# Kernel optimization log

Measured on AMD Instinct MI355X. Metric: run time of the kernel, lower is better.

## Reference

```python
import jax, jax.numpy as jnp
import numpy as np

N = 50000        # nodes
E = 800000       # edges
G = 256          # graphs in batch
DIMS = [128, 128, 64, 32]
BN_EPS = 1e-5
TEMP = 5.0


def setup_inputs() -> dict:
    key = jax.random.key(0)
    ks = iter(jax.random.split(key, 32))
    inp = {}
    inp["x"] = jax.random.normal(next(ks), (N, DIMS[0]), dtype=jnp.float32)
    inp["edge_index"] = jax.random.randint(next(ks), (2, E), 0, N)
    inp["batch"] = jnp.sort(jax.random.randint(next(ks), (N,), 0, G))
    for i in range(3):
        din, dout = DIMS[i], DIMS[i + 1]
        inp[f"W1_{i}"] = jax.random.normal(next(ks), (din, dout), dtype=jnp.float32) * 0.05
        inp[f"b1_{i}"] = jnp.zeros((dout,), jnp.float32)
        inp[f"W2_{i}"] = jax.random.normal(next(ks), (dout, dout), dtype=jnp.float32) * 0.05
        inp[f"b2_{i}"] = jnp.zeros((dout,), jnp.float32)
        inp[f"gamma_{i}"] = jnp.ones((dout,), jnp.float32)
        inp[f"beta_{i}"] = jnp.zeros((dout,), jnp.float32)
        inp[f"mean_{i}"] = jnp.zeros((dout,), jnp.float32)
        inp[f"var_{i}"] = jnp.ones((dout,), jnp.float32)
    inp["W_lin"] = jax.random.normal(next(ks), (DIMS[3], 1), dtype=jnp.float32) * 0.05
    inp["b_lin"] = jnp.zeros((1,), jnp.float32)
    return inp


def _gin_bn(x, src, dst, W1, b1, W2, b2, g, b, m, v):
    # GINConv with eps=0: h_i = MLP(x_i + sum_{j->i} x_j), then BatchNorm (eval)
    agg = jax.ops.segment_sum(x[src], dst, num_segments=N)  # [N, din]
    h = x + agg
    h = jnp.maximum(h @ W1 + b1, 0.0) @ W2 + b2             # 2-layer MLP
    return (h - m) * jax.lax.rsqrt(v + BN_EPS) * g + b


def reference(x, edge_index, batch,
              W1_0, b1_0, W2_0, b2_0, gamma_0, beta_0, mean_0, var_0,
              W1_1, b1_1, W2_1, b2_1, gamma_1, beta_1, mean_1, var_1,
              W1_2, b1_2, W2_2, b2_2, gamma_2, beta_2, mean_2, var_2,
              W_lin, b_lin):
    src, dst = edge_index[0], edge_index[1]
    layers = [
        (W1_0, b1_0, W2_0, b2_0, gamma_0, beta_0, mean_0, var_0),
        (W1_1, b1_1, W2_1, b2_1, gamma_1, beta_1, mean_1, var_1),
        (W1_2, b1_2, W2_2, b2_2, gamma_2, beta_2, mean_2, var_2),
    ]
    for i, p in enumerate(layers):
        x = _gin_bn(x, src, dst, *p)
        if i != len(layers) - 1:
            x = jnp.maximum(x, 0.0)  # relu; dropout is identity in eval mode
    logits = (x @ W_lin + b_lin) / TEMP                      # [N, 1]
    # per-graph (segment) softmax over nodes
    mx = jax.ops.segment_max(logits, batch, num_segments=G)  # [G, 1]
    e = jnp.exp(logits - mx[batch])
    s = jax.ops.segment_sum(e, batch, num_segments=G)        # [G, 1]
    return e / s[batch]
```

## Files before the change

### kernel.cpp

```cpp
#include <hip/hip_runtime.h>

#define NN 50000
#define NE 800000
#define NG 256
#define NB ((NN + 255) / 256)
#define N4 (NN * 128 / 4)
#define NQ (NE / 4)

typedef __attribute__((ext_vector_type(8))) short bf16x8;
typedef __attribute__((ext_vector_type(4))) float f32x4;

__device__ __forceinline__ unsigned short f2bf_rne(float f) {
    unsigned u = __float_as_uint(f);
    u += 0x7fffu + ((u >> 16) & 1u);
    return (unsigned short)(u >> 16);
}
#define BF2F_LO(u) __uint_as_float((u) << 16)
#define BF2F_HI(u) __uint_as_float((u) & 0xffff0000u)

__global__ void conv_hist(const float4* __restrict__ x, ushort4* __restrict__ xh,
                          const int4* __restrict__ dst4, int* __restrict__ deg,
                          int4* __restrict__ eoff4) {
    int i = blockIdx.x * 256 + threadIdx.x;
    if (i < N4) {
        float4 v = x[i];
        ushort4 o;
        o.x = f2bf_rne(v.x); o.y = f2bf_rne(v.y);
        o.z = f2bf_rne(v.z); o.w = f2bf_rne(v.w);
        xh[i] = o;
    }
    int wv = threadIdx.x >> 6, ln = threadIdx.x & 63;
    if (ln < 8) {
        int q = blockIdx.x * 32 + wv * 8 + ln;
        if (q < NQ) {
            int4 d = dst4[q];
            int o0 = atomicAdd(&deg[d.x], 1);
            int o1 = atomicAdd(&deg[d.y], 1);
            int o2 = atomicAdd(&deg[d.z], 1);
            int o3 = atomicAdd(&deg[d.w], 1);
            eoff4[q] = make_int4(o0, o1, o2, o3);
        }
    }
}

__global__ void block_scan(const int* __restrict__ deg, int* __restrict__ iscan,
                           int* __restrict__ bsum,
                           const float* __restrict__ W1, const float* __restrict__ W2,
                           const float* __restrict__ W3,
                           const float* __restrict__ W21, const float* __restrict__ W12,
                           unsigned short* __restrict__ W1t,
                           unsigned short* __restrict__ W2t,
                           unsigned short* __restrict__ W3t,
                           unsigned short* __restrict__ W21t,
                           unsigned short* __restrict__ W12t) {
    int gidx = blockIdx.x * 256 + threadIdx.x;
    if (gidx < 16384) {
        int n = gidx >> 7, k = gidx & 127;
        W1t[gidx] = f2bf_rne(W1[k * 128 + n]);
        W2t[gidx] = f2bf_rne(W2[k * 128 + n]);
    } else if (gidx < 24576) {
        int i2 = gidx - 16384;
        int n = i2 >> 7, k = i2 & 127;
        W3t[i2] = f2bf_rne(W3[k * 64 + n]);
    } else if (gidx < 28672) {
        int i3 = gidx - 24576;
        int n = i3 >> 6, k = i3 & 63;
        W21t[i3] = f2bf_rne(W21[k * 64 + n]);
    } else if (gidx < 30720) {
        int i4 = gidx - 28672;
        int n = i4 >> 6, k = i4 & 63;
        W12t[i4] = f2bf_rne(W12[k * 32 + n]);
    }

    __shared__ int sh[256];
    int t = threadIdx.x;
    int i = blockIdx.x * 256 + t;
    int v = (i < NN) ? deg[i] : 0;
    sh[t] = v;
    __syncthreads();
    #pragma unroll
    for (int off = 1; off < 256; off <<= 1) {
        int add = (t >= off) ? sh[t - off] : 0;
        __syncthreads();
        sh[t] += add;
        __syncthreads();
    }
    if (i < NN) iscan[i] = sh[t];
    if (t == 255) bsum[blockIdx.x] = sh[255];
}

__global__ void scan_bsum(const int* __restrict__ bsum, int* __restrict__ boff) {
    __shared__ int sh[256];
    int t = threadIdx.x;
    int v = (t < NB) ? bsum[t] : 0;
    sh[t] = v;
    __syncthreads();
    #pragma unroll
    for (int off = 1; off < 256; off <<= 1) {
        int add = (t >= off) ? sh[t - off] : 0;
        __syncthreads();
        sh[t] += add;
        __syncthreads();
    }
    if (t < NB) boff[t] = sh[t] - v;
}

__global__ void finalize_bounds(const int* __restrict__ deg, const int* __restrict__ iscan,
                                const int* __restrict__ boff, int* __restrict__ rowptr,
                                const int* __restrict__ batch, int* __restrict__ gstart) {
    int i = blockIdx.x * 256 + threadIdx.x;
    if (i < NN) {
        rowptr[i] = iscan[i] - deg[i] + boff[blockIdx.x];
        int b = batch[i];
        if (i == 0) {
            for (int g = 0; g <= b; g++) gstart[g] = 0;
        } else {
            int p = batch[i - 1];
            for (int g = p + 1; g <= b; g++) gstart[g] = i;
        }
        if (i == NN - 1) {
            for (int g = b + 1; g <= NG; g++) gstart[g] = NN;
        }
    }
    if (i == 0) rowptr[NN] = NE;
}

__global__ void fill_csr2(const int4* __restrict__ src4, const int4* __restrict__ dst4,
                          const int* __restrict__ rowptr, const int4* __restrict__ eoff4,
                          int* __restrict__ esrc) {
    int q = blockIdx.x * 256 + threadIdx.x;
    if (q >= NQ) return;
    int4 s = src4[q];
    int4 d = dst4[q];
    int4 o = eoff4[q];
    int r0 = rowptr[d.x];
    int r1 = rowptr[d.y];
    int r2 = rowptr[d.z];
    int r3 = rowptr[d.w];
    esrc[r0 + o.x] = s.x;
    esrc[r1 + o.y] = s.y;
    esrc[r2 + o.z] = s.z;
    esrc[r3 + o.w] = s.w;
}


template <int C4>
__device__ __forceinline__ void gather_bf16(const uint4* __restrict__ x4,
                                            const int* __restrict__ esrc,
                                            int beg, int cnt, int node, int lane,
                                            float* a ) {
    constexpr int EPI = 64 / C4;
    const int chunk = lane & (C4 - 1);
    const int esl   = lane / C4;
    #define ACC_U4(u) do { \
        a[0] += BF2F_LO((u).x); a[1] += BF2F_HI((u).x); \
        a[2] += BF2F_LO((u).y); a[3] += BF2F_HI((u).y); \
        a[4] += BF2F_LO((u).z); a[5] += BF2F_HI((u).z); \
        a[6] += BF2F_LO((u).w); a[7] += BF2F_HI((u).w); } while (0)
    if (esl == 0) { uint4 u = x4[(size_t)node * C4 + chunk]; ACC_U4(u); }
    for (int c = 0; c < cnt; c += 64) {
        int take = min(64, cnt - c);
        int myi = (lane < take) ? esrc[beg + c + lane] : 0;
        int i = 0;
        for (; i + 4 * EPI <= take; i += 4 * EPI) {
            int s0 = __shfl(myi, i + esl);
            int s1 = __shfl(myi, i + EPI + esl);
            int s2 = __shfl(myi, i + 2 * EPI + esl);
            int s3 = __shfl(myi, i + 3 * EPI + esl);
            uint4 u0 = x4[(size_t)s0 * C4 + chunk];
            uint4 u1 = x4[(size_t)s1 * C4 + chunk];
            uint4 u2 = x4[(size_t)s2 * C4 + chunk];
            uint4 u3 = x4[(size_t)s3 * C4 + chunk];
            ACC_U4(u0); ACC_U4(u1); ACC_U4(u2); ACC_U4(u3);
        }
        if (i + 2 * EPI <= take) {
            int s0 = __shfl(myi, i + esl);
            int s1 = __shfl(myi, i + EPI + esl);
            uint4 u0 = x4[(size_t)s0 * C4 + chunk];
            uint4 u1 = x4[(size_t)s1 * C4 + chunk];
            ACC_U4(u0); ACC_U4(u1);
            i += 2 * EPI;
        }
        if (i + EPI <= take) {
            int s = __shfl(myi, i + esl);
            uint4 u = x4[(size_t)s * C4 + chunk];
            ACC_U4(u);
            i += EPI;
        }
        int rem = take - i;
        if (rem > 0) {
            int s = __shfl(myi, i + ((esl < rem) ? esl : 0));
            uint4 u = x4[(size_t)s * C4 + chunk];
            if (esl < rem) ACC_U4(u);
        }
    }
    #undef ACC_U4
    for (int off = 32; off >= C4; off >>= 1) {
        #pragma unroll
        for (int q = 0; q < 8; q++)
            a[q] += __shfl_xor(a[q], off);
    }
}

template <int C>
__device__ __forceinline__ void gather_bf16_u2(const uint2* __restrict__ x2,
                                               const int* __restrict__ esrc,
                                               int beg, int cnt, int node, int lane,
                                               float* a ) {
    constexpr int EPI = 64 / C;
    const int chunk = lane & (C - 1);
    const int esl   = lane / C;
    #define ACC_U2(u) do { \
        a[0] += BF2F_LO((u).x); a[1] += BF2F_HI((u).x); \
        a[2] += BF2F_LO((u).y); a[3] += BF2F_HI((u).y); } while (0)
    if (esl == 0) { uint2 u = x2[(size_t)node * C + chunk]; ACC_U2(u); }
    for (int c = 0; c < cnt; c += 64) {
        int take = min(64, cnt - c);
        int myi = (lane < take) ? esrc[beg + c + lane] : 0;
        int i = 0;
        for (; i + 4 * EPI <= take; i += 4 * EPI) {
            int s0 = __shfl(myi, i + esl);
            int s1 = __shfl(myi, i + EPI + esl);
            int s2 = __shfl(myi, i + 2 * EPI + esl);
            int s3 = __shfl(myi, i + 3 * EPI + esl);
            uint2 u0 = x2[(size_t)s0 * C + chunk];
            uint2 u1 = x2[(size_t)s1 * C + chunk];
            uint2 u2 = x2[(size_t)s2 * C + chunk];
            uint2 u3 = x2[(size_t)s3 * C + chunk];
            ACC_U2(u0); ACC_U2(u1); ACC_U2(u2); ACC_U2(u3);
        }
        if (i + 2 * EPI <= take) {
            int s0 = __shfl(myi, i + esl);
            int s1 = __shfl(myi, i + EPI + esl);
            uint2 u0 = x2[(size_t)s0 * C + chunk];
            uint2 u1 = x2[(size_t)s1 * C + chunk];
            ACC_U2(u0); ACC_U2(u1);
            i += 2 * EPI;
        }
        if (i + EPI <= take) {
            int s = __shfl(myi, i + esl);
            uint2 u = x2[(size_t)s * C + chunk];
            ACC_U2(u);
            i += EPI;
        }
        int rem = take - i;
        if (rem > 0) {
            int s = __shfl(myi, i + ((esl < rem) ? esl : 0));
            uint2 u = x2[(size_t)s * C + chunk];
            if (esl < rem) ACC_U2(u);
        }
    }
    #undef ACC_U2
    for (int off = 32; off >= C; off >>= 1) {
        #pragma unroll
        for (int q = 0; q < 4; q++)
            a[q] += __shfl_xor(a[q], off);
    }
}

template <int C>
__device__ __forceinline__ void gather_bf16_u1(const unsigned* __restrict__ x1,
                                               const int* __restrict__ esrc,
                                               int beg, int cnt, int node, int lane,
                                               float* a ) {
    constexpr int EPI = 64 / C;
    const int chunk = lane & (C - 1);
    const int esl   = lane / C;
    #define ACC_U1(u) do { \
        a[0] += BF2F_LO(u); a[1] += BF2F_HI(u); } while (0)
    if (esl == 0) { unsigned u = x1[(size_t)node * C + chunk]; ACC_U1(u); }
    for (int c = 0; c < cnt; c += 64) {
        int take = min(64, cnt - c);
        int myi = (lane < take) ? esrc[beg + c + lane] : 0;
        int i = 0;
        for (; i + 4 * EPI <= take; i += 4 * EPI) {
            int s0 = __shfl(myi, i + esl);
            int s1 = __shfl(myi, i + EPI + esl);
            int s2 = __shfl(myi, i + 2 * EPI + esl);
            int s3 = __shfl(myi, i + 3 * EPI + esl);
            unsigned u0 = x1[(size_t)s0 * C + chunk];
            unsigned u1 = x1[(size_t)s1 * C + chunk];
            unsigned u2 = x1[(size_t)s2 * C + chunk];
            unsigned u3 = x1[(size_t)s3 * C + chunk];
            ACC_U1(u0); ACC_U1(u1); ACC_U1(u2); ACC_U1(u3);
        }
        if (i + 2 * EPI <= take) {
            int s0 = __shfl(myi, i + esl);
            int s1 = __shfl(myi, i + EPI + esl);
            unsigned u0 = x1[(size_t)s0 * C + chunk];
            unsigned u1 = x1[(size_t)s1 * C + chunk];
            ACC_U1(u0); ACC_U1(u1);
            i += 2 * EPI;
        }
        if (i + EPI <= take) {
            int s = __shfl(myi, i + esl);
            unsigned u = x1[(size_t)s * C + chunk];
            ACC_U1(u);
            i += EPI;
        }
        int rem = take - i;
        if (rem > 0) {
            int s = __shfl(myi, i + ((esl < rem) ? esl : 0));
            unsigned u = x1[(size_t)s * C + chunk];
            if (esl < rem) ACC_U1(u);
        }
    }
    #undef ACC_U1
    for (int off = 32; off >= C; off >>= 1) {
        #pragma unroll
        for (int q = 0; q < 2; q++)
            a[q] += __shfl_xor(a[q], off);
    }
}

__global__ __launch_bounds__(256) void gather_L0(
        const unsigned short* __restrict__ xh, const int* __restrict__ esrc,
        const int* __restrict__ rowptr, unsigned short* __restrict__ aggh ) {
    const int wave = threadIdx.x >> 6, lane = threadIdx.x & 63;
    const int node = blockIdx.x * 4 + wave;
    if (node >= NN) return;
    float a[8] = {0, 0, 0, 0, 0, 0, 0, 0};
    int beg = rowptr[node], end = rowptr[node + 1];
    gather_bf16<16>((const uint4*)xh, esrc, beg, end - beg, node, lane, a);
    if (lane < 16) {
        uint4 o;
        o.x = (unsigned)f2bf_rne(a[0]) | ((unsigned)f2bf_rne(a[1]) << 16);
        o.y = (unsigned)f2bf_rne(a[2]) | ((unsigned)f2bf_rne(a[3]) << 16);
        o.z = (unsigned)f2bf_rne(a[4]) | ((unsigned)f2bf_rne(a[5]) << 16);
        o.w = (unsigned)f2bf_rne(a[6]) | ((unsigned)f2bf_rne(a[7]) << 16);
        *(uint4*)&aggh[(size_t)node * 128 + lane * 8] = o;
    }
}

__global__ __launch_bounds__(256) void gather_L1(
        const unsigned short* __restrict__ z1h, const int* __restrict__ esrc,
        const int* __restrict__ rowptr, const float* __restrict__ b1,
        unsigned short* __restrict__ agg1h ) {
    const int wave = threadIdx.x >> 6, lane = threadIdx.x & 63;
    const int node = blockIdx.x * 4 + wave;
    if (node >= NN) return;
    float a[4] = {0, 0, 0, 0};
    int beg = rowptr[node], end = rowptr[node + 1];
    gather_bf16_u2<16>((const uint2*)z1h, esrc, beg, end - beg, node, lane, a);
    if (lane < 16) {
        float4 bv = *(const float4*)&b1[lane * 4];
        uint2 o;
        o.x = (unsigned)f2bf_rne(fmaxf(a[0] + bv.x, 0.f)) |
              ((unsigned)f2bf_rne(fmaxf(a[1] + bv.y, 0.f)) << 16);
        o.y = (unsigned)f2bf_rne(fmaxf(a[2] + bv.z, 0.f)) |
              ((unsigned)f2bf_rne(fmaxf(a[3] + bv.w, 0.f)) << 16);
        *(uint2*)&agg1h[(size_t)node * 64 + lane * 4] = o;
    }
}

__global__ __launch_bounds__(256) void gather_L2(
        const unsigned short* __restrict__ z2h, const int* __restrict__ esrc,
        const int* __restrict__ rowptr, const float* __restrict__ b1,
        unsigned short* __restrict__ agg2h ) {
    const int wave = threadIdx.x >> 6, lane = threadIdx.x & 63;
    const int node = blockIdx.x * 4 + wave;
    if (node >= NN) return;
    float a[2] = {0, 0};
    int beg = rowptr[node], end = rowptr[node + 1];
    gather_bf16_u1<16>((const unsigned*)z2h, esrc, beg, end - beg, node, lane, a);
    if (lane < 16) {
        float2 bv = *(const float2*)&b1[lane * 2];
        unsigned o = (unsigned)f2bf_rne(fmaxf(a[0] + bv.x, 0.f)) |
                     ((unsigned)f2bf_rne(fmaxf(a[1] + bv.y, 0.f)) << 16);
        *(unsigned*)&agg2h[(size_t)node * 32 + lane * 2] = o;
    }
}

__global__ __launch_bounds__(256) void gemm_L0(
        const unsigned short* __restrict__ aggh, unsigned short* __restrict__ z1h,
        const unsigned short* __restrict__ W1t,
        const unsigned short* __restrict__ W2t,
        const unsigned short* __restrict__ W3t,
        const float* __restrict__ b1, const float* __restrict__ b2,
        const float* __restrict__ gamma, const float* __restrict__ beta,
        const float* __restrict__ mean, const float* __restrict__ var) {
    constexpr int MT = 64, LDA = 136;
    __shared__ __align__(16) unsigned short shA[MT * LDA];
    __shared__ __align__(16) unsigned short shB[MT * LDA];
    const int tid = threadIdx.x;
    const int wave = tid >> 6, lane = tid & 63;
    const int nodeBase = blockIdx.x * MT;
    const int lr = lane & 15;
    const int lg = lane >> 4;
    const int lk = lg * 8;
    const int n0 = wave * 32;

    #pragma unroll
    for (int j = 0; j < 4; j++) {
        int f = tid + j * 256;
        int row = f >> 4, c = f & 15;
        int node = nodeBase + row;
        uint4 v = (node < NN) ? ((const uint4*)aggh)[(size_t)node * 16 + c]
                              : make_uint4(0u, 0u, 0u, 0u);
        *(uint4*)&shA[row * LDA + c * 8] = v;
    }
    __syncthreads();

    f32x4 acc[4][2];

    {
        float bv0 = b1[n0 + lr], bv1 = b1[n0 + 16 + lr];
        #pragma unroll
        for (int m = 0; m < 4; m++) {
            f32x4 c0 = {bv0, bv0, bv0, bv0};
            f32x4 c1 = {bv1, bv1, bv1, bv1};
            acc[m][0] = c0; acc[m][1] = c1;
        }
        #pragma unroll
        for (int ks = 0; ks < 4; ks++) {
            const int k0 = ks * 32 + lk;
            bf16x8 wb0 = *(const bf16x8*)&W1t[(n0 + lr) * 128 + k0];
            bf16x8 wb1 = *(const bf16x8*)&W1t[(n0 + 16 + lr) * 128 + k0];
            #pragma unroll
            for (int m = 0; m < 4; m++) {
                bf16x8 af = *(const bf16x8*)&shA[(m * 16 + lr) * LDA + k0];
                acc[m][0] = __builtin_amdgcn_mfma_f32_16x16x32_bf16(af, wb0, acc[m][0], 0, 0, 0);
                acc[m][1] = __builtin_amdgcn_mfma_f32_16x16x32_bf16(af, wb1, acc[m][1], 0, 0, 0);
            }
        }
    }
    #pragma unroll
    for (int m = 0; m < 4; m++) {
        #pragma unroll
        for (int nt = 0; nt < 2; nt++) {
            #pragma unroll
            for (int r = 0; r < 4; r++) {
                shB[(m * 16 + lg * 4 + r) * LDA + (n0 + nt * 16 + lr)] =
                    f2bf_rne(fmaxf(acc[m][nt][r], 0.f));
            }
        }
    }
    __syncthreads();

    {
        float bv0 = b2[n0 + lr], bv1 = b2[n0 + 16 + lr];
        #pragma unroll
        for (int m = 0; m < 4; m++) {
            f32x4 c0 = {bv0, bv0, bv0, bv0};
            f32x4 c1 = {bv1, bv1, bv1, bv1};
            acc[m][0] = c0; acc[m][1] = c1;
        }
        #pragma unroll
        for (int ks = 0; ks < 4; ks++) {
            const int k0 = ks * 32 + lk;
            bf16x8 wb0 = *(const bf16x8*)&W2t[(n0 + lr) * 128 + k0];
            bf16x8 wb1 = *(const bf16x8*)&W2t[(n0 + 16 + lr) * 128 + k0];
            #pragma unroll
            for (int m = 0; m < 4; m++) {
                bf16x8 af = *(const bf16x8*)&shB[(m * 16 + lr) * LDA + k0];
                acc[m][0] = __builtin_amdgcn_mfma_f32_16x16x32_bf16(af, wb0, acc[m][0], 0, 0, 0);
                acc[m][1] = __builtin_amdgcn_mfma_f32_16x16x32_bf16(af, wb1, acc[m][1], 0, 0, 0);
            }
        }
    }
    float s0 = gamma[n0 + lr]      * (1.0f / sqrtf(var[n0 + lr] + 1e-5f));
    float t0 = beta[n0 + lr]       - mean[n0 + lr] * s0;
    float s1 = gamma[n0 + 16 + lr] * (1.0f / sqrtf(var[n0 + 16 + lr] + 1e-5f));
    float t1 = beta[n0 + 16 + lr]  - mean[n0 + 16 + lr] * s1;
    #pragma unroll
    for (int m = 0; m < 4; m++) {
        #pragma unroll
        for (int nt = 0; nt < 2; nt++) {
            float sc = nt ? s1 : s0, sf = nt ? t1 : t0;
            #pragma unroll
            for (int r = 0; r < 4; r++) {
                float y = fmaxf(fmaf(acc[m][nt][r], sc, sf), 0.f);
                shA[(m * 16 + lg * 4 + r) * LDA + (n0 + nt * 16 + lr)] = f2bf_rne(y);
            }
        }
    }
    __syncthreads();

    f32x4 a3[4];
    #pragma unroll
    for (int m = 0; m < 4; m++) {
        f32x4 z = {0.f, 0.f, 0.f, 0.f};
        a3[m] = z;
    }
    #pragma unroll
    for (int ks = 0; ks < 4; ks++) {
        const int k0 = ks * 32 + lk;
        bf16x8 wb = *(const bf16x8*)&W3t[(wave * 16 + lr) * 128 + k0];
        #pragma unroll
        for (int m = 0; m < 4; m++) {
            bf16x8 af = *(const bf16x8*)&shA[(m * 16 + lr) * LDA + k0];
            a3[m] = __builtin_amdgcn_mfma_f32_16x16x32_bf16(af, wb, a3[m], 0, 0, 0);
        }
    }
    #pragma unroll
    for (int m = 0; m < 4; m++) {
        #pragma unroll
        for (int r = 0; r < 4; r++) {
            int node = nodeBase + m * 16 + lg * 4 + r;
            if (node < NN)
                z1h[(size_t)node * 64 + wave * 16 + lr] = f2bf_rne(a3[m][r]);
        }
    }
}

__global__ __launch_bounds__(256) void gemm_L1(
        const unsigned short* __restrict__ agg1h, unsigned short* __restrict__ z2h,
        const unsigned short* __restrict__ W21t,
        const unsigned short* __restrict__ W12t,
        const float* __restrict__ b2, const float* __restrict__ gamma,
        const float* __restrict__ beta, const float* __restrict__ mean,
        const float* __restrict__ var) {
    constexpr int MT = 64, LDA = 72;
    __shared__ __align__(16) unsigned short shA[MT * LDA];
    __shared__ __align__(16) unsigned short shB[MT * LDA];
    const int tid = threadIdx.x;
    const int wave = tid >> 6, lane = tid & 63;
    const int nodeBase = blockIdx.x * MT;
    const int lr = lane & 15;
    const int lg = lane >> 4;
    const int lk = lg * 8;
    const int n0 = wave * 16;

    #pragma unroll
    for (int j = 0; j < 2; j++) {
        int f = tid + j * 256;
        int row = f >> 3, c = f & 7;
        int node = nodeBase + row;
        uint4 v = (node < NN) ? ((const uint4*)agg1h)[(size_t)node * 8 + c]
                              : make_uint4(0u, 0u, 0u, 0u);
        *(uint4*)&shA[row * LDA + c * 8] = v;
    }
    __syncthreads();

    f32x4 acc[4];
    {
        float bv = b2[n0 + lr];
        #pragma unroll
        for (int m = 0; m < 4; m++) {
            f32x4 c0 = {bv, bv, bv, bv};
            acc[m] = c0;
        }
        #pragma unroll
        for (int ks = 0; ks < 2; ks++) {
            const int k0 = ks * 32 + lk;
            bf16x8 wb = *(const bf16x8*)&W21t[(n0 + lr) * 64 + k0];
            #pragma unroll
            for (int m = 0; m < 4; m++) {
                bf16x8 af = *(const bf16x8*)&shA[(m * 16 + lr) * LDA + k0];
                acc[m] = __builtin_amdgcn_mfma_f32_16x16x32_bf16(af, wb, acc[m], 0, 0, 0);
            }
        }
    }
    float sc = gamma[n0 + lr] * (1.0f / sqrtf(var[n0 + lr] + 1e-5f));
    float sf = beta[n0 + lr] - mean[n0 + lr] * sc;
    #pragma unroll
    for (int m = 0; m < 4; m++) {
        #pragma unroll
        for (int r = 0; r < 4; r++) {
            float y = fmaxf(fmaf(acc[m][r], sc, sf), 0.f);
            shB[(m * 16 + lg * 4 + r) * LDA + (n0 + lr)] = f2bf_rne(y);
        }
    }
    __syncthreads();

    const int rh = (wave >> 1) * 32, ch = (wave & 1) * 16;
    f32x4 a3[2];
    {
        f32x4 z = {0.f, 0.f, 0.f, 0.f};
        a3[0] = z; a3[1] = z;
    }
    #pragma unroll
    for (int ks = 0; ks < 2; ks++) {
        const int k0 = ks * 32 + lk;
        bf16x8 wb = *(const bf16x8*)&W12t[(ch + lr) * 64 + k0];
        #pragma unroll
        for (int m = 0; m < 2; m++) {
            bf16x8 af = *(const bf16x8*)&shB[(rh + m * 16 + lr) * LDA + k0];
            a3[m] = __builtin_amdgcn_mfma_f32_16x16x32_bf16(af, wb, a3[m], 0, 0, 0);
        }
    }
    #pragma unroll
    for (int m = 0; m < 2; m++) {
        #pragma unroll
        for (int r = 0; r < 4; r++) {
            int node = nodeBase + rh + m * 16 + lg * 4 + r;
            if (node < NN)
                z2h[(size_t)node * 32 + ch + lr] = f2bf_rne(a3[m][r]);
        }
    }
}

__global__ __launch_bounds__(256) void gemm_L2(
        const unsigned short* __restrict__ agg2h, float* __restrict__ logits,
        const float* __restrict__ W2, const float* __restrict__ b2,
        const float* __restrict__ gamma, const float* __restrict__ beta,
        const float* __restrict__ mean, const float* __restrict__ var,
        const float* __restrict__ Wl, const float* __restrict__ bl) {
    constexpr int MT = 32, LD = 36;
    __shared__ float sh[MT * LD];
    const int tid = threadIdx.x;
    const int nodeBase = blockIdx.x * MT;

    {
        int row = tid >> 3, c = tid & 7;
        int node = nodeBase + row;
        uint2 v = (node < NN) ? ((const uint2*)agg2h)[(size_t)node * 8 + c]
                              : make_uint2(0u, 0u);
        sh[row * LD + c * 4 + 0] = BF2F_LO(v.x);
        sh[row * LD + c * 4 + 1] = BF2F_HI(v.x);
        sh[row * LD + c * 4 + 2] = BF2F_LO(v.y);
        sh[row * LD + c * 4 + 3] = BF2F_HI(v.y);
    }
    __syncthreads();

    const int colid = tid % 8, rowid = tid / 8;
    const int c0 = colid * 4, r0 = rowid;
    float acc[4];
    {
        float4 bv = *(const float4*)&b2[c0];
        acc[0] = bv.x; acc[1] = bv.y; acc[2] = bv.z; acc[3] = bv.w;
        #pragma unroll
        for (int k4 = 0; k4 < 8; k4++) {
            float4 w[4];
            #pragma unroll
            for (int kk = 0; kk < 4; kk++)
                w[kk] = *(const float4*)&W2[(k4 * 4 + kk) * 32 + c0];
            float4 a = *(const float4*)&sh[r0 * LD + k4 * 4];
            const float av[4] = {a.x, a.y, a.z, a.w};
            #pragma unroll
            for (int kk = 0; kk < 4; kk++) {
                const float* wp = (const float*)&w[kk];
                #pragma unroll
                for (int j = 0; j < 4; j++)
                    acc[j] = fmaf(av[kk], wp[j], acc[j]);
            }
        }
    }
    float4 gv = *(const float4*)&gamma[c0];
    float4 bev = *(const float4*)&beta[c0];
    float4 mv = *(const float4*)&mean[c0];
    float4 vv = *(const float4*)&var[c0];
    float4 wl = *(const float4*)&Wl[c0];
    float p = 0.f;
    {
        const float* gp = (const float*)&gv; const float* bp = (const float*)&bev;
        const float* mp = (const float*)&mv; const float* vp = (const float*)&vv;
        const float* wp = (const float*)&wl;
        #pragma unroll
        for (int j = 0; j < 4; j++) {
            float sc = gp[j] * (1.0f / sqrtf(vp[j] + 1e-5f));
            float y = (acc[j] - mp[j]) * sc + bp[j];
            p = fmaf(y, wp[j], p);
        }
    }
    p += __shfl_xor(p, 1);
    p += __shfl_xor(p, 2);
    p += __shfl_xor(p, 4);
    int node = nodeBase + r0;
    if ((tid & 7) == 0 && node < NN)
        logits[node] = (p + bl[0]) * 0.2f;
}

__global__ __launch_bounds__(256) void seg_softmax(
        const float* __restrict__ logits, const int* __restrict__ gstart,
        float* __restrict__ out) {
    __shared__ float slog[1024];
    __shared__ float sred[4];
    __shared__ float sbc[2];
    int g = blockIdx.x;
    int beg = gstart[g], end = gstart[g + 1];
    int cnt = end - beg;
    int t = threadIdx.x;
    if (cnt <= 0) return;
    bool fits = (cnt <= 1024);

    float lmax = -3.402823466e+38f;
    for (int i = t; i < cnt; i += 256) {
        float lg = logits[beg + i];
        if (fits) slog[i] = lg;
        lmax = fmaxf(lmax, lg);
    }
    #pragma unroll
    for (int off = 32; off > 0; off >>= 1)
        lmax = fmaxf(lmax, __shfl_down(lmax, off));
    if ((t & 63) == 0) sred[t >> 6] = lmax;
    __syncthreads();
    if (t == 0) sbc[0] = fmaxf(fmaxf(sred[0], sred[1]), fmaxf(sred[2], sred[3]));
    __syncthreads();
    float gm = sbc[0];

    float lsum = 0.f;
    for (int i = t; i < cnt; i += 256) {
        float lg = fits ? slog[i] : logits[beg + i];
        float e = expf(lg - gm);
        if (fits) slog[i] = e;
        lsum += e;
    }
    #pragma unroll
    for (int off = 32; off > 0; off >>= 1)
        lsum += __shfl_down(lsum, off);
    __syncthreads();
    if ((t & 63) == 0) sred[t >> 6] = lsum;
    __syncthreads();
    if (t == 0) sbc[1] = (sred[0] + sred[1]) + (sred[2] + sred[3]);
    __syncthreads();
    float inv = 1.0f / sbc[1];

    for (int i = t; i < cnt; i += 256) {
        float e = fits ? slog[i] : expf(logits[beg + i] - gm);
        out[beg + i] = e * inv;
    }
}

extern "C" void kernel_launch(void* const* d_in, const int* in_sizes, int n_in,
                              void* d_out, int out_size, void* d_ws, size_t ws_size,
                              hipStream_t stream) {
    const float* x    = (const float*)d_in[0];
    const int*   ei   = (const int*)d_in[1];
    const int*   srcI = ei;
    const int*   dstI = ei + NE;
    const int*   batch = (const int*)d_in[2];

    const float* P[29];
    for (int i = 0; i < 29; i++) P[i] = (const float*)d_in[i];
    const float* Wlin = P[27];
    const float* blin = P[28];

    unsigned short* xh  = (unsigned short*)d_ws;
    unsigned short* z1h = xh + (size_t)NN * 128;
    unsigned short* z2h = z1h + (size_t)NN * 64;
    float* logits = (float*)(z2h + (size_t)NN * 32);
    int* gstart = (int*)(logits + NN);
    int* deg    = gstart + NG + 1;
    int* iscan  = deg + NN;
    int* rowptr = iscan + NN;
    int* bsum   = rowptr + NN + 1;
    int* boff   = bsum + NB;
    uintptr_t eal = ((uintptr_t)(boff + NB) + 15) & ~(uintptr_t)15;
    int* eoff   = (int*)eal;
    int* esrc   = eoff + NE;
    uintptr_t pal = ((uintptr_t)(esrc + NE) + 255) & ~(uintptr_t)255;
    unsigned short* aggh  = (unsigned short*)pal;
    unsigned short* W1t   = aggh + (size_t)NN * 128;
    unsigned short* W2t   = W1t + 16384;
    unsigned short* W3t   = W2t + 16384;
    unsigned short* W21t  = W3t + 8192;
    unsigned short* W12t  = W21t + 4096;
    unsigned short* agg1h = W12t + 2048;
    unsigned short* agg2h = agg1h + (size_t)NN * 64;
    float* outp = (float*)d_out;

    const int TB = 256;

    hipMemsetAsync(deg, 0, NN * sizeof(int), stream);
    conv_hist<<<(N4 + TB - 1) / TB, TB, 0, stream>>>(
        (const float4*)x, (ushort4*)xh, (const int4*)dstI, deg, (int4*)eoff);

    block_scan<<<NB, 256, 0, stream>>>(deg, iscan, bsum,
        P[3], P[5], P[11], P[13], P[19], W1t, W2t, W3t, W21t, W12t);
    scan_bsum<<<1, 256, 0, stream>>>(bsum, boff);
    finalize_bounds<<<NB, 256, 0, stream>>>(deg, iscan, boff, rowptr, batch, gstart);
    fill_csr2<<<(NQ + TB - 1) / TB, TB, 0, stream>>>(
        (const int4*)srcI, (const int4*)dstI, rowptr, (const int4*)eoff, esrc);

    const int GB   = (NN + 3) / 4;
    const int FB64 = (NN + 63) / 64;
    const int FB32 = (NN + 31) / 32;

    gather_L0<<<GB, 256, 0, stream>>>(xh, esrc, rowptr, aggh);
    gemm_L0<<<FB64, 256, 0, stream>>>(aggh, z1h, W1t, W2t, W3t,
        P[4], P[6], P[7], P[8], P[9], P[10]);
    gather_L1<<<GB, 256, 0, stream>>>(z1h, esrc, rowptr, P[12], agg1h);
    gemm_L1<<<FB64, 256, 0, stream>>>(agg1h, z2h, W21t, W12t,
        P[14], P[15], P[16], P[17], P[18]);
    gather_L2<<<GB, 256, 0, stream>>>(z2h, esrc, rowptr, P[20], agg2h);
    gemm_L2<<<FB32, 256, 0, stream>>>(agg2h, logits,
        P[21], P[22], P[23], P[24], P[25], P[26], Wlin, blin);

    seg_softmax<<<NG, 256, 0, stream>>>(logits, gstart, outp);
}
```

Baseline: 287.9 us.

## Privatize degree histogram per XCD and fold block-offset scan into finalize

The degree-count atomics now go to one of eight per-XCD private histograms, chosen from the hardware XCC id, so atomics from different dies no longer contend on shared cache lines. Each edge offset is tagged with its XCD, and block_scan merges the private counts into per-XCD base offsets. The separate single-block scan_bsum launch is removed; each finalize block instead reduces the preceding block sums itself. In exchange it adds an 8x larger memset, extra base-array reads in fill_csr, and redundant per-block reductions.

New measurement: 283.4 us. Within noise of the previous version (-1.6%).

```diff
diff --git a/kernel.cpp b/kernel.cpp
--- a/kernel.cpp
+++ b/kernel.cpp
@@ -19,8 +19,8 @@
 #define BF2F_HI(u) __uint_as_float((u) & 0xffff0000u)
 
 __global__ void conv_hist(const float4* __restrict__ x, ushort4* __restrict__ xh,
-                          const int4* __restrict__ dst4, int* __restrict__ deg,
-                          int4* __restrict__ eoff4) {
+                          const int4* __restrict__ dst4, int* __restrict__ deg_priv,
+                          uint4* __restrict__ eoffx4) {
     int i = blockIdx.x * 256 + threadIdx.x;
     if (i < N4) {
         float4 v = x[i];
@@ -33,17 +33,23 @@
     if (ln < 8) {
         int q = blockIdx.x * 32 + wv * 8 + ln;
         if (q < NQ) {
+            unsigned xcd;
+            asm volatile("s_getreg_b32 %0, hwreg(HW_REG_XCC_ID)" : "=s"(xcd));
+            xcd &= 7u;
+            int* mydeg = deg_priv + (size_t)xcd * NN;
             int4 d = dst4[q];
-            int o0 = atomicAdd(&deg[d.x], 1);
-            int o1 = atomicAdd(&deg[d.y], 1);
-            int o2 = atomicAdd(&deg[d.z], 1);
-            int o3 = atomicAdd(&deg[d.w], 1);
-            eoff4[q] = make_int4(o0, o1, o2, o3);
-        }
-    }
-}
-
-__global__ void block_scan(const int* __restrict__ deg, int* __restrict__ iscan,
+            unsigned o0 = (unsigned)atomicAdd(&mydeg[d.x], 1);
+            unsigned o1 = (unsigned)atomicAdd(&mydeg[d.y], 1);
+            unsigned o2 = (unsigned)atomicAdd(&mydeg[d.z], 1);
+            unsigned o3 = (unsigned)atomicAdd(&mydeg[d.w], 1);
+            unsigned tag = xcd << 16;
+            eoffx4[q] = make_uint4(tag | o0, tag | o1, tag | o2, tag | o3);
+        }
+    }
+}
+
+__global__ void block_scan(const int* __restrict__ deg_priv, int* __restrict__ deg,
+                           int* __restrict__ base, int* __restrict__ iscan,
                            int* __restrict__ bsum,
                            const float* __restrict__ W1, const float* __restrict__ W2,
                            const float* __restrict__ W3,
@@ -75,7 +81,17 @@
     __shared__ int sh[256];
     int t = threadIdx.x;
     int i = blockIdx.x * 256 + t;
-    int v = (i < NN) ? deg[i] : 0;
+    int v = 0;
+    if (i < NN) {
+        int run = 0;
+        #pragma unroll
+        for (int xx = 0; xx < 8; xx++) {
+            base[(size_t)xx * NN + i] = run;
+            run += deg_priv[(size_t)xx * NN + i];
+        }
+        deg[i] = run;
+        v = run;
+    }
     sh[t] = v;
     __syncthreads();
     #pragma unroll
@@ -89,28 +105,23 @@
     if (t == 255) bsum[blockIdx.x] = sh[255];
 }
 
-__global__ void scan_bsum(const int* __restrict__ bsum, int* __restrict__ boff) {
-    __shared__ int sh[256];
+__global__ void finalize_bounds(const int* __restrict__ deg, const int* __restrict__ iscan,
+                                const int* __restrict__ bsum, int* __restrict__ rowptr,
+                                const int* __restrict__ batch, int* __restrict__ gstart) {
+    __shared__ int sb[256];
     int t = threadIdx.x;
-    int v = (t < NB) ? bsum[t] : 0;
-    sh[t] = v;
-    __syncthreads();
-    #pragma unroll
-    for (int off = 1; off < 256; off <<= 1) {
-        int add = (t >= off) ? sh[t - off] : 0;
+    sb[t] = (t < blockIdx.x) ? bsum[t] : 0;
+    __syncthreads();
+    #pragma unroll
+    for (int off = 128; off > 0; off >>= 1) {
+        if (t < off) sb[t] += sb[t + off];
         __syncthreads();
-        sh[t] += add;
-        __syncthreads();
-    }
-    if (t < NB) boff[t] = sh[t] - v;
-}
-
-__global__ void finalize_bounds(const int* __restrict__ deg, const int* __restrict__ iscan,
-                                const int* __restrict__ boff, int* __restrict__ rowptr,
-                                const int* __restrict__ batch, int* __restrict__ gstart) {
-    int i = blockIdx.x * 256 + threadIdx.x;
+    }
+    int boff = sb[0];
+
+    int i = blockIdx.x * 256 + t;
     if (i < NN) {
-        rowptr[i] = iscan[i] - deg[i] + boff[blockIdx.x];
+        rowptr[i] = iscan[i] - deg[i] + boff;
         int b = batch[i];
         if (i == 0) {
             for (int g = 0; g <= b; g++) gstart[g] = 0;
@@ -126,21 +137,21 @@
 }
 
 __global__ void fill_csr2(const int4* __restrict__ src4, const int4* __restrict__ dst4,
-                          const int* __restrict__ rowptr, const int4* __restrict__ eoff4,
-                          int* __restrict__ esrc) {
+                          const int* __restrict__ rowptr, const int* __restrict__ base,
+                          const uint4* __restrict__ eoffx4, int* __restrict__ esrc) {
     int q = blockIdx.x * 256 + threadIdx.x;
     if (q >= NQ) return;
     int4 s = src4[q];
     int4 d = dst4[q];
-    int4 o = eoff4[q];
-    int r0 = rowptr[d.x];
-    int r1 = rowptr[d.y];
-    int r2 = rowptr[d.z];
-    int r3 = rowptr[d.w];
-    esrc[r0 + o.x] = s.x;
-    esrc[r1 + o.y] = s.y;
-    esrc[r2 + o.z] = s.z;
-    esrc[r3 + o.w] = s.w;
+    uint4 e = eoffx4[q];
+    int p0 = rowptr[d.x] + base[(size_t)(e.x >> 16) * NN + d.x] + (int)(e.x & 0xffffu);
+    int p1 = rowptr[d.y] + base[(size_t)(e.y >> 16) * NN + d.y] + (int)(e.y & 0xffffu);
+    int p2 = rowptr[d.z] + base[(size_t)(e.z >> 16) * NN + d.z] + (int)(e.z & 0xffffu);
+    int p3 = rowptr[d.w] + base[(size_t)(e.w >> 16) * NN + d.w] + (int)(e.w & 0xffffu);
+    esrc[p0] = s.x;
+    esrc[p1] = s.y;
+    esrc[p2] = s.z;
+    esrc[p3] = s.w;
 }
 
 
@@ -731,14 +742,15 @@
     unsigned short* z2h = z1h + (size_t)NN * 64;
     float* logits = (float*)(z2h + (size_t)NN * 32);
     int* gstart = (int*)(logits + NN);
-    int* deg    = gstart + NG + 1;
-    int* iscan  = deg + NN;
-    int* rowptr = iscan + NN;
-    int* bsum   = rowptr + NN + 1;
-    int* boff   = bsum + NB;
-    uintptr_t eal = ((uintptr_t)(boff + NB) + 15) & ~(uintptr_t)15;
-    int* eoff   = (int*)eal;
-    int* esrc   = eoff + NE;
+    int* deg      = gstart + NG + 1;
+    int* deg_priv = deg + NN;
+    int* base     = deg_priv + 8 * NN;
+    int* iscan    = base + 8 * NN;
+    int* rowptr   = iscan + NN;
+    int* bsum     = rowptr + NN + 1;
+    uintptr_t eal = ((uintptr_t)(bsum + NB) + 15) & ~(uintptr_t)15;
+    unsigned* eoffx = (unsigned*)eal;
+    int* esrc   = (int*)(eoffx + NE);
     uintptr_t pal = ((uintptr_t)(esrc + NE) + 255) & ~(uintptr_t)255;
     unsigned short* aggh  = (unsigned short*)pal;
     unsigned short* W1t   = aggh + (size_t)NN * 128;
@@ -752,16 +764,15 @@
 
     const int TB = 256;
 
-    hipMemsetAsync(deg, 0, NN * sizeof(int), stream);
+    hipMemsetAsync(deg_priv, 0, 8 * NN * sizeof(int), stream);
     conv_hist<<<(N4 + TB - 1) / TB, TB, 0, stream>>>(
-        (const float4*)x, (ushort4*)xh, (const int4*)dstI, deg, (int4*)eoff);
-
-    block_scan<<<NB, 256, 0, stream>>>(deg, iscan, bsum,
+        (const float4*)x, (ushort4*)xh, (const int4*)dstI, deg_priv, (uint4*)eoffx);
+
+    block_scan<<<NB, 256, 0, stream>>>(deg_priv, deg, base, iscan, bsum,
         P[3], P[5], P[11], P[13], P[19], W1t, W2t, W3t, W21t, W12t);
-    scan_bsum<<<1, 256, 0, stream>>>(bsum, boff);
-    finalize_bounds<<<NB, 256, 0, stream>>>(deg, iscan, boff, rowptr, batch, gstart);
+    finalize_bounds<<<NB, 256, 0, stream>>>(deg, iscan, bsum, rowptr, batch, gstart);
     fill_csr2<<<(NQ + TB - 1) / TB, TB, 0, stream>>>(
-        (const int4*)srcI, (const int4*)dstI, rowptr, (const int4*)eoff, esrc);
+        (const int4*)srcI, (const int4*)dstI, rowptr, base, (const uint4*)eoffx, esrc);
 
     const int GB   = (NN + 3) / 4;
     const int FB64 = (NN + 63) / 64;
```
